# Performance work log

Hardware: AMD Instinct MI355X
Metric: run time of the kernel (lower is better)

## Reference

```python
import jax, jax.numpy as jnp
import numpy as np
from jax import lax

B, T, H, W, D = 4, 24, 32, 32, 128
N_CONV = 5            # 32 -> 1 via five stride-2 convs
NUM_FREQS = T // 2    # 12
N_EXPERTS = 7         # unique int periods of rfftfreq(24)[1:]
TOP_K = 2
BN_EPS = 1e-5
COMBINE_EPS = float(np.finfo(np.float64).eps)


def setup_inputs() -> dict:
    key = jax.random.key(0)
    ks = jax.random.split(key, 12)
    x = jax.random.normal(ks[0], (B, T, H, W, D), jnp.float32)
    conv_w = jax.random.normal(ks[1], (N_CONV, D, D, 2, 2), jnp.float32) / np.sqrt(4 * D)
    conv_b = jax.random.normal(ks[2], (N_CONV, D), jnp.float32) * 0.1
    bn_gamma = jax.random.uniform(ks[3], (N_CONV, D), jnp.float32, 0.5, 1.5)
    bn_beta = jax.random.normal(ks[4], (N_CONV, D), jnp.float32) * 0.1
    bn_mean = jax.random.normal(ks[5], (N_CONV, D), jnp.float32) * 0.1
    bn_var = jax.random.uniform(ks[6], (N_CONV, D), jnp.float32, 0.5, 1.5)
    fuse_w = jax.random.normal(ks[7], (D, 1), jnp.float32) / np.sqrt(D)
    fuse_b = jax.random.normal(ks[8], (1,), jnp.float32) * 0.1
    w_gate = jax.random.normal(ks[9], (NUM_FREQS, N_EXPERTS), jnp.float32)
    expert_w = jax.random.normal(ks[10], (N_EXPERTS, D, D), jnp.float32) / np.sqrt(D)
    expert_b = jax.random.normal(ks[11], (N_EXPERTS, D), jnp.float32) * 0.1
    return dict(x=x, conv_w=conv_w, conv_b=conv_b, bn_gamma=bn_gamma, bn_beta=bn_beta,
                bn_mean=bn_mean, bn_var=bn_var, fuse_w=fuse_w, fuse_b=fuse_b,
                w_gate=w_gate, expert_w=expert_w, expert_b=expert_b, top_k=TOP_K)


def _gates(x, conv_w, conv_b, bn_gamma, bn_beta, bn_mean, bn_var, fuse_w, fuse_b, w_gate, top_k):
    b, t, h, w, d = x.shape
    # (b t h w d) -> (bt, d, h, w)
    z = jnp.transpose(x.reshape(b * t, h, w, d), (0, 3, 1, 2))
    for i in range(conv_w.shape[0]):  # fixed small layer loop
        z = lax.conv_general_dilated(z, conv_w[i], (2, 2), 'VALID',
                                     dimension_numbers=('NCHW', 'OIHW', 'NCHW'))
        z = z + conv_b[i][None, :, None, None]
        z = bn_gamma[i][None, :, None, None] * (z - bn_mean[i][None, :, None, None]) \
            * lax.rsqrt(bn_var[i][None, :, None, None] + BN_EPS) + bn_beta[i][None, :, None, None]
        z = jnp.where(z > 0, z, 0.2 * z)  # LeakyReLU(0.2)
    hh, ww = z.shape[-2], z.shape[-1]
    # (bt, d, h, w) -> (b, t, h*w*d)  matching einops '(b t) d h w -> b t (h w d)'
    z = jnp.transpose(z.reshape(b, t, d, hh, ww), (0, 1, 3, 4, 2)).reshape(b, t, hh * ww * d)
    s = (z @ fuse_w + fuse_b)[..., 0]  # [B, T]
    xf = jnp.fft.rfft(s, axis=-1, norm='ortho')[:, 1:]  # drop DC -> [B, T//2]
    amp = jnp.abs(xf)
    logits = amp @ w_gate  # [B, E]  (eval path: no noise)
    top_vals, top_idx = lax.top_k(logits, top_k + 1)
    tk_vals, tk_idx = top_vals[:, :top_k], top_idx[:, :top_k]
    tk_gates = jax.nn.softmax(tk_vals, axis=-1)
    gates = jnp.zeros_like(logits).at[jnp.arange(b)[:, None], tk_idx].set(tk_gates)
    return gates


def reference(x, conv_w, conv_b, bn_gamma, bn_beta, bn_mean, bn_var,
              fuse_w, fuse_b, w_gate, expert_w, expert_b, top_k):
    gates = _gates(x, conv_w, conv_b, bn_gamma, bn_beta, bn_mean, bn_var,
                   fuse_w, fuse_b, w_gate, top_k)  # [B, E]
    # Dense equivalent of dispatch -> per-expert linear -> combine:
    # combine does exp(expert_out), gate-weighted scatter-add over batch, then log.
    expert_out = jnp.einsum('bthwd,edf->bethwf', x, expert_w) \
                 + expert_b[None, :, None, None, None, :]  # [B,E,T,H,W,D]
    combined = jnp.einsum('be,bethwf->bthwf', gates, jnp.exp(expert_out))
    combined = jnp.where(combined == 0, COMBINE_EPS, combined)
    return jnp.log(combined)
```

## Files before the change

### kernel.cpp

```cpp
#include <hip/hip_runtime.h>
#include <hip/hip_bf16.h>

#define D_ 128
#define T_ 24
#define NPB 24576

typedef __attribute__((ext_vector_type(8))) short bf16x8;
typedef __attribute__((ext_vector_type(4))) float f32x4;
typedef unsigned short ushortt;

static __device__ __forceinline__ void load8(const float* p, float* dst){
  float4 a = *(const float4*)p; float4 b = *(const float4*)(p+4);
  dst[0]=a.x;dst[1]=a.y;dst[2]=a.z;dst[3]=a.w;dst[4]=b.x;dst[5]=b.y;dst[6]=b.z;dst[7]=b.w;
}
static __device__ __forceinline__ bf16x8 cvt8(const float* f){
  union { bf16x8 v; __hip_bfloat162 h[4]; } u;
#pragma unroll
  for (int i=0;i<4;i++) u.h[i] = __float22bfloat162_rn(make_float2(f[2*i], f[2*i+1]));
  return u.v;
}
static __device__ __forceinline__ void split8(const float* f, bf16x8* hh, bf16x8* ll){
  union { bf16x8 v; __hip_bfloat162 h[4]; } uh, ul;
  float lo[8];
#pragma unroll
  for (int i=0;i<4;i++){
    __hip_bfloat162 p = __float22bfloat162_rn(make_float2(f[2*i], f[2*i+1]));
    uh.h[i] = p;
    lo[2*i]   = f[2*i]   - __bfloat162float(p.x);
    lo[2*i+1] = f[2*i+1] - __bfloat162float(p.y);
  }
#pragma unroll
  for (int i=0;i<4;i++) ul.h[i] = __float22bfloat162_rn(make_float2(lo[2*i], lo[2*i+1]));
  *hh = uh.v; *ll = ul.v;
}

__global__ void prep_frags(const float* __restrict__ cw, const float* __restrict__ ew,
                           ushortt* __restrict__ wfC, ushortt* __restrict__ wfE, int do_e)
{
  const int idx = blockIdx.x*256 + threadIdx.x;
  if (idx < 10240){
    const int l  = idx >> 11;
    const int n  = (idx >> 4) & 127;
    const int k8 = (idx & 15) * 8;
    const float* src = cw + (size_t)((l*128 + n)*128 + k8)*4;
    float4 v[8];
#pragma unroll
    for (int kk=0;kk<8;++kk) v[kk] = *(const float4*)&src[kk*4];
    const int fk = k8>>5, q = (k8>>3)&3, ng = n>>4;
    const int lanoff = (q*16 + (n&15))*8;
#pragma unroll
    for (int tap=0; tap<4; ++tap){
      float f[8];
#pragma unroll
      for (int kk=0;kk<8;++kk) f[kk] = ((const float*)&v[kk])[tap];
      bf16x8 hh, ll; split8(f, &hh, &ll);
      *(bf16x8*)&wfC[(size_t)((((l*4+tap)*2+0)*4+fk)*8+ng)*512 + lanoff] = hh;
      *(bf16x8*)&wfC[(size_t)((((l*4+tap)*2+1)*4+fk)*8+ng)*512 + lanoff] = ll;
    }
  } else if (do_e && idx < 10240 + 14336){
    const int j  = idx - 10240;
    const int e  = j >> 11;
    const int n  = (j >> 4) & 127;
    const int k8 = (j & 15) * 8;
    float f[8];
#pragma unroll
    for (int kk=0;kk<8;++kk) f[kk] = ew[(size_t)(e*128 + k8+kk)*128 + n];
    const int fk = k8>>5, q = (k8>>3)&3, ng = n>>4;
    *(bf16x8*)&wfE[(size_t)((e*4+fk)*8+ng)*512 + (q*16 + (n&15))*8] = cvt8(f);
  }
}

template<int MG>
__global__ __launch_bounds__(256, 4)
void conv3(const float* __restrict__ in, float* __restrict__ out,
           const ushortt* __restrict__ wf,
           const float* __restrict__ cb,  const float* __restrict__ gam,
           const float* __restrict__ bet, const float* __restrict__ mn,
           const float* __restrict__ vr,  int n_pix, int lw)
{
  const int t = threadIdx.x;
  const int w = t>>6, lane = t&63, quad = lane>>4, l16 = lane&15;
  const int nh = w*32;
  const int row0 = blockIdx.x*(MG*16);
  const int Win = 2<<lw;
  int inb[MG];
#pragma unroll
  for (int mg=0; mg<MG; ++mg){
    const int p = row0 + mg*16 + l16;
    const int n   = p >> (2*lw);
    const int rem = p - (n << (2*lw));
    const int oy  = rem >> lw, ox = rem - (oy<<lw);
    inb[mg] = ((n*Win  + 2*oy)*Win + 2*ox) << 7;
  }
  f32x4 acc[MG][2];
#pragma unroll
  for (int mg=0;mg<MG;++mg){ acc[mg][0]=(f32x4){0,0,0,0}; acc[mg][1]=acc[mg][0]; }

#pragma unroll
  for (int tap=0; tap<4; ++tap){
    const int toff = (((tap>>1)*Win) + (tap&1)) << 7;
#pragma unroll
    for (int fk=0; fk<4; ++fk){
      bf16x8 ah[MG], al[MG];
#pragma unroll
      for (int mg=0; mg<MG; ++mg){
        float f[8]; load8(in + inb[mg] + toff + fk*32 + quad*8, f);
        split8(f, &ah[mg], &al[mg]);
      }
#pragma unroll
      for (int ngl=0; ngl<2; ++ngl){
        const int ng = w*2 + ngl;
        const bf16x8 bh = *(const bf16x8*)&wf[(size_t)(((tap*2+0)*4+fk)*8+ng)*512 + lane*8];
        const bf16x8 bl = *(const bf16x8*)&wf[(size_t)(((tap*2+1)*4+fk)*8+ng)*512 + lane*8];
#pragma unroll
        for (int mg=0; mg<MG; ++mg){
          acc[mg][ngl] = __builtin_amdgcn_mfma_f32_16x16x32_bf16(ah[mg], bh, acc[mg][ngl], 0,0,0);
          acc[mg][ngl] = __builtin_amdgcn_mfma_f32_16x16x32_bf16(ah[mg], bl, acc[mg][ngl], 0,0,0);
          acc[mg][ngl] = __builtin_amdgcn_mfma_f32_16x16x32_bf16(al[mg], bh, acc[mg][ngl], 0,0,0);
        }
      }
    }
  }
#pragma unroll
  for (int ngl=0; ngl<2; ++ngl){
    const int col = nh + ngl*16 + l16;
    const float sc  = gam[col]*rsqrtf(vr[col]+1e-5f);
    const float cbv = cb[col], bt = bet[col], mv = mn[col];
#pragma unroll
    for (int mg=0; mg<MG; ++mg)
#pragma unroll
      for (int r=0; r<4; ++r){
        const int pix = row0 + mg*16 + quad*4 + r;
        float v = acc[mg][ngl][r] + cbv;
        v = sc*(v - mv) + bt;
        out[(size_t)pix*D_ + col] = v>0.f ? v : 0.2f*v;
      }
  }
}

__global__ void gate_kernel(const float* __restrict__ z, const float* __restrict__ fw,
                            const float* __restrict__ fb, const float* __restrict__ wg,
                            float* __restrict__ gbuf)
{
  __shared__ float s[96];
  __shared__ float amp[4][12];
  __shared__ float logits[4][7];
  const int t = threadIdx.x;
  if (t < 96){
    float a = 0.f;
    for (int d=0; d<D_; d++) a = fmaf(z[t*D_+d], fw[d], a);
    s[t] = a + fb[0];
  }
  __syncthreads();
  if (t < 48){
    const int b = t / 12, kf = (t % 12) + 1;
    float re=0.f, im=0.f;
    for (int tt=0; tt<T_; tt++){
      int ph = (kf*tt) % T_;
      float ang = (float)ph * (6.283185307179586f / (float)T_);
      re = fmaf(s[b*T_+tt], cosf(ang), re);
      im = fmaf(s[b*T_+tt], sinf(ang), im);
    }
    amp[b][t%12] = sqrtf(re*re + im*im) * 0.20412414523193150f;
  }
  __syncthreads();
  if (t < 28){
    const int b = t/7, e = t - (t/7)*7;
    float a = 0.f;
    for (int k=0;k<12;k++) a = fmaf(amp[b][k], wg[k*7+e], a);
    logits[b][e] = a;
  }
  __syncthreads();
  if (t < 4){
    const int b = t;
    int i0=0; float v0=logits[b][0];
    for (int e=1;e<7;e++){ float v=logits[b][e]; if (v > v0){ v0=v; i0=e; } }
    int i1=-1; float v1=-3.4e38f;
    for (int e=0;e<7;e++){ if (e==i0) continue; float v=logits[b][e]; if (v > v1){ v1=v; i1=e; } }
    float ed = expf(v1 - v0);
    gbuf[b*4+0] = 1.f/(1.f+ed);
    gbuf[b*4+1] = ed/(1.f+ed);
    ((int*)gbuf)[b*4+2] = i0;
    ((int*)gbuf)[b*4+3] = i1;
  }
}

template<bool WF>
__global__ __launch_bounds__(256, 3)
void expert3(const float* __restrict__ x, const float* __restrict__ ew,
             const ushortt* __restrict__ wfe, const float* __restrict__ eb,
             const float* __restrict__ gbuf, float* __restrict__ outp)
{
  __shared__ ushortt wlds[WF ? 16 : 32768];
  const int t = threadIdx.x;
  const int w = t>>6, lane = t&63, quad = lane>>4, l16 = lane&15;
  const int nh = w*32;
  const size_t row0 = (size_t)blockIdx.x * 64;
  const int b = (int)(row0 / NPB);
  const float g0 = gbuf[b*4+0], g1 = gbuf[b*4+1];
  const int e0 = ((const int*)gbuf)[b*4+2];
  const int e1 = ((const int*)gbuf)[b*4+3];

  if (!WF){
    const int el = t>>7, r7 = t&127;
    const int n0 = (r7&31)*4, k0 = (r7>>5)*16;
    const int esel = el ? e1 : e0;
#pragma unroll
    for (int h=0; h<2; ++h)
#pragma unroll
      for (int sub=0; sub<2; ++sub){
        const int kb = h*64 + k0 + sub*8;
        float4 v[8];
#pragma unroll
        for (int kk=0;kk<8;++kk)
          v[kk] = *(const float4*)&ew[(size_t)esel*16384 + (size_t)(kb+kk)*D_ + n0];
        const int fk = kb>>5, q = (kb>>3)&3;
#pragma unroll
        for (int n=0;n<4;++n){
          float f[8];
#pragma unroll
          for (int kk=0;kk<8;++kk) f[kk] = ((const float*)&v[kk])[n];
          *(bf16x8*)&wlds[(size_t)(((el*4+fk)*8 + ((n0+n)>>4))*512 + (q*16 + ((n0+n)&15))*8)] = cvt8(f);
        }
      }
    __syncthreads();
  }

  f32x4 acc[2][4][2];
#pragma unroll
  for (int e=0;e<2;++e)
#pragma unroll
    for (int mg=0;mg<4;++mg){ acc[e][mg][0]=(f32x4){0,0,0,0}; acc[e][mg][1]=acc[e][mg][0]; }

#pragma unroll
  for (int fk=0; fk<4; ++fk){
    bf16x8 a[4];
#pragma unroll
    for (int mg=0; mg<4; ++mg){
      float f[8]; load8(x + (row0 + mg*16 + l16)*D_ + fk*32 + quad*8, f);
      a[mg] = cvt8(f);
    }
#pragma unroll
    for (int e=0; e<2; ++e){
      const int eg = e ? e1 : e0;
#pragma unroll
      for (int ngl=0; ngl<2; ++ngl){
        const int ng = w*2 + ngl;
        bf16x8 bb;
        if (WF) bb = *(const bf16x8*)&wfe[(size_t)((eg*4+fk)*8+ng)*512 + lane*8];
        else    bb = *(const bf16x8*)&wlds[(size_t)((e*4+fk)*8+ng)*512 + lane*8];
#pragma unroll
        for (int mg=0; mg<4; ++mg)
          acc[e][mg][ngl] = __builtin_amdgcn_mfma_f32_16x16x32_bf16(a[mg], bb, acc[e][mg][ngl], 0,0,0);
      }
    }
  }
#pragma unroll
  for (int ngl=0; ngl<2; ++ngl){
    const int col = nh + ngl*16 + l16;
    const float be0 = eb[e0*D_ + col];
    const float be1 = eb[e1*D_ + col];
#pragma unroll
    for (int mg=0; mg<4; ++mg)
#pragma unroll
      for (int r=0; r<4; ++r){
        const size_t row = row0 + mg*16 + quad*4 + r;
        float c = g0*__expf(acc[0][mg][ngl][r] + be0) + g1*__expf(acc[1][mg][ngl][r] + be1);
        if (c == 0.f) c = 2.220446049250313e-16f;
        outp[row*D_ + col] = __logf(c);
      }
  }
}

extern "C" void kernel_launch(void* const* d_in, const int* in_sizes, int n_in,
                              void* d_out, int out_size, void* d_ws, size_t ws_size,
                              hipStream_t stream)
{
  const float* x   = (const float*)d_in[0];
  const float* cw  = (const float*)d_in[1];
  const float* cb  = (const float*)d_in[2];
  const float* gam = (const float*)d_in[3];
  const float* bet = (const float*)d_in[4];
  const float* mn  = (const float*)d_in[5];
  const float* vr  = (const float*)d_in[6];
  const float* fw  = (const float*)d_in[7];
  const float* fb  = (const float*)d_in[8];
  const float* wg  = (const float*)d_in[9];
  const float* ew  = (const float*)d_in[10];
  const float* eb  = (const float*)d_in[11];
  float* out = (float*)d_out;

  char* sb = (char*)d_out;
  ushortt* wfC = (ushortt*)sb;
  float* bufA  = (float*)(sb + 1310720);
  float* bufB  = (float*)(sb + 13893632);
  float* zbuf  = (float*)(sb + 17039360);
  float* gbuf  = (float*)d_ws;

  const bool use_wf = ws_size >= (size_t)(64 + 7*4*8*512*2);
  ushortt* wfE = use_wf ? (ushortt*)((char*)d_ws + 64) : wfC ;

  prep_frags<<<96, 256, 0, stream>>>(cw, ew, wfC, wfE, use_wf ? 1 : 0);
  conv3<2><<<768, 256, 0, stream>>>(x,    bufA, wfC,          cb,     gam,     bet,     mn,     vr,     24576, 4);
  conv3<2><<<192, 256, 0, stream>>>(bufA, bufB, wfC + 131072, cb+128, gam+128, bet+128, mn+128, vr+128,  6144, 3);
  conv3<1><<< 96, 256, 0, stream>>>(bufB, bufA, wfC + 262144, cb+256, gam+256, bet+256, mn+256, vr+256,  1536, 2);
  conv3<1><<< 24, 256, 0, stream>>>(bufA, bufB, wfC + 393216, cb+384, gam+384, bet+384, mn+384, vr+384,   384, 1);
  conv3<1><<<  6, 256, 0, stream>>>(bufB, zbuf, wfC + 524288, cb+512, gam+512, bet+512, mn+512, vr+512,    96, 0);
  gate_kernel<<<1, 128, 0, stream>>>(zbuf, fw, fb, wg, gbuf);
  if (use_wf) expert3<true ><<<1536, 256, 0, stream>>>(x, ew, wfE, eb, gbuf, out);
  else        expert3<false><<<1536, 256, 0, stream>>>(x, ew, wfE, eb, gbuf, out);
}
```

Before: 223.0 us.

## Fuse all stages into one cooperative persistent kernel with grid syncs

After: 222.9 us. Within noise of the previous version (-0.0%).

```diff
diff --git a/kernel.cpp b/kernel.cpp
--- a/kernel.cpp
+++ b/kernel.cpp
@@ -1,5 +1,8 @@
 #include <hip/hip_runtime.h>
 #include <hip/hip_bf16.h>
+#include <hip/hip_cooperative_groups.h>
+
+namespace cg = cooperative_groups;
 
 #define D_ 128
 #define T_ 24
@@ -34,10 +37,10 @@
   *hh = uh.v; *ll = ul.v;
 }
 
-__global__ void prep_frags(const float* __restrict__ cw, const float* __restrict__ ew,
-                           ushortt* __restrict__ wfC, ushortt* __restrict__ wfE, int do_e)
-{
-  const int idx = blockIdx.x*256 + threadIdx.x;
+static __device__ __forceinline__ void prep_body(const float* __restrict__ cw,
+    const float* __restrict__ ew, ushortt* __restrict__ wfC, ushortt* __restrict__ wfE,
+    int do_e, int idx)
+{
   if (idx < 10240){
     const int l  = idx >> 11;
     const int n  = (idx >> 4) & 127;
@@ -70,6 +73,78 @@
   }
 }
 
+__global__ void prep_frags(const float* __restrict__ cw, const float* __restrict__ ew,
+                           ushortt* __restrict__ wfC, ushortt* __restrict__ wfE, int do_e)
+{
+  prep_body(cw, ew, wfC, wfE, do_e, blockIdx.x*256 + threadIdx.x);
+}
+
+template<int MG>
+static __device__ __forceinline__ void conv_body(const float* __restrict__ in,
+           float* __restrict__ out, const ushortt* __restrict__ wf,
+           const float* __restrict__ cb,  const float* __restrict__ gam,
+           const float* __restrict__ bet, const float* __restrict__ mn,
+           const float* __restrict__ vr,  int row0, int lw)
+{
+  const int t = threadIdx.x;
+  const int w = t>>6, lane = t&63, quad = lane>>4, l16 = lane&15;
+  const int nh = w*32;
+  const int Win = 2<<lw;
+  int inb[MG];
+#pragma unroll
+  for (int mg=0; mg<MG; ++mg){
+    const int p = row0 + mg*16 + l16;
+    const int n   = p >> (2*lw);
+    const int rem = p - (n << (2*lw));
+    const int oy  = rem >> lw, ox = rem - (oy<<lw);
+    inb[mg] = ((n*Win  + 2*oy)*Win + 2*ox) << 7;
+  }
+  f32x4 acc[MG][2];
+#pragma unroll
+  for (int mg=0;mg<MG;++mg){ acc[mg][0]=(f32x4){0,0,0,0}; acc[mg][1]=acc[mg][0]; }
+
+#pragma unroll
+  for (int tap=0; tap<4; ++tap){
+    const int toff = (((tap>>1)*Win) + (tap&1)) << 7;
+#pragma unroll
+    for (int fk=0; fk<4; ++fk){
+      bf16x8 ah[MG], al[MG];
+#pragma unroll
+      for (int mg=0; mg<MG; ++mg){
+        float f[8]; load8(in + inb[mg] + toff + fk*32 + quad*8, f);
+        split8(f, &ah[mg], &al[mg]);
+      }
+#pragma unroll
+      for (int ngl=0; ngl<2; ++ngl){
+        const int ng = w*2 + ngl;
+        const bf16x8 bh = *(const bf16x8*)&wf[(size_t)(((tap*2+0)*4+fk)*8+ng)*512 + lane*8];
+        const bf16x8 bl = *(const bf16x8*)&wf[(size_t)(((tap*2+1)*4+fk)*8+ng)*512 + lane*8];
+#pragma unroll
+        for (int mg=0; mg<MG; ++mg){
+          acc[mg][ngl] = __builtin_amdgcn_mfma_f32_16x16x32_bf16(ah[mg], bh, acc[mg][ngl], 0,0,0);
+          acc[mg][ngl] = __builtin_amdgcn_mfma_f32_16x16x32_bf16(ah[mg], bl, acc[mg][ngl], 0,0,0);
+          acc[mg][ngl] = __builtin_amdgcn_mfma_f32_16x16x32_bf16(al[mg], bh, acc[mg][ngl], 0,0,0);
+        }
+      }
+    }
+  }
+#pragma unroll
+  for (int ngl=0; ngl<2; ++ngl){
+    const int col = nh + ngl*16 + l16;
+    const float sc  = gam[col]*rsqrtf(vr[col]+1e-5f);
+    const float cbv = cb[col], bt = bet[col], mv = mn[col];
+#pragma unroll
+    for (int mg=0; mg<MG; ++mg)
+#pragma unroll
+      for (int r=0; r<4; ++r){
+        const int pix = row0 + mg*16 + quad*4 + r;
+        float v = acc[mg][ngl][r] + cbv;
+        v = sc*(v - mv) + bt;
+        out[(size_t)pix*D_ + col] = v>0.f ? v : 0.2f*v;
+      }
+  }
+}
+
 template<int MG>
 __global__ __launch_bounds__(256, 4)
 void conv3(const float* __restrict__ in, float* __restrict__ out,
@@ -78,69 +153,13 @@
            const float* __restrict__ bet, const float* __restrict__ mn,
            const float* __restrict__ vr,  int n_pix, int lw)
 {
-  const int t = threadIdx.x;
-  const int w = t>>6, lane = t&63, quad = lane>>4, l16 = lane&15;
-  const int nh = w*32;
-  const int row0 = blockIdx.x*(MG*16);
-  const int Win = 2<<lw;
-  int inb[MG];
-#pragma unroll
-  for (int mg=0; mg<MG; ++mg){
-    const int p = row0 + mg*16 + l16;
-    const int n   = p >> (2*lw);
-    const int rem = p - (n << (2*lw));
-    const int oy  = rem >> lw, ox = rem - (oy<<lw);
-    inb[mg] = ((n*Win  + 2*oy)*Win + 2*ox) << 7;
-  }
-  f32x4 acc[MG][2];
-#pragma unroll
-  for (int mg=0;mg<MG;++mg){ acc[mg][0]=(f32x4){0,0,0,0}; acc[mg][1]=acc[mg][0]; }
-
-#pragma unroll
-  for (int tap=0; tap<4; ++tap){
-    const int toff = (((tap>>1)*Win) + (tap&1)) << 7;
-#pragma unroll
-    for (int fk=0; fk<4; ++fk){
-      bf16x8 ah[MG], al[MG];
-#pragma unroll
-      for (int mg=0; mg<MG; ++mg){
-        float f[8]; load8(in + inb[mg] + toff + fk*32 + quad*8, f);
-        split8(f, &ah[mg], &al[mg]);
-      }
-#pragma unroll
-      for (int ngl=0; ngl<2; ++ngl){
-        const int ng = w*2 + ngl;
-        const bf16x8 bh = *(const bf16x8*)&wf[(size_t)(((tap*2+0)*4+fk)*8+ng)*512 + lane*8];
-        const bf16x8 bl = *(const bf16x8*)&wf[(size_t)(((tap*2+1)*4+fk)*8+ng)*512 + lane*8];
-#pragma unroll
-        for (int mg=0; mg<MG; ++mg){
-          acc[mg][ngl] = __builtin_amdgcn_mfma_f32_16x16x32_bf16(ah[mg], bh, acc[mg][ngl], 0,0,0);
-          acc[mg][ngl] = __builtin_amdgcn_mfma_f32_16x16x32_bf16(ah[mg], bl, acc[mg][ngl], 0,0,0);
-          acc[mg][ngl] = __builtin_amdgcn_mfma_f32_16x16x32_bf16(al[mg], bh, acc[mg][ngl], 0,0,0);
-        }
-      }
-    }
-  }
-#pragma unroll
-  for (int ngl=0; ngl<2; ++ngl){
-    const int col = nh + ngl*16 + l16;
-    const float sc  = gam[col]*rsqrtf(vr[col]+1e-5f);
-    const float cbv = cb[col], bt = bet[col], mv = mn[col];
-#pragma unroll
-    for (int mg=0; mg<MG; ++mg)
-#pragma unroll
-      for (int r=0; r<4; ++r){
-        const int pix = row0 + mg*16 + quad*4 + r;
-        float v = acc[mg][ngl][r] + cbv;
-        v = sc*(v - mv) + bt;
-        out[(size_t)pix*D_ + col] = v>0.f ? v : 0.2f*v;
-      }
-  }
-}
-
-__global__ void gate_kernel(const float* __restrict__ z, const float* __restrict__ fw,
-                            const float* __restrict__ fb, const float* __restrict__ wg,
-                            float* __restrict__ gbuf)
+  (void)n_pix;
+  conv_body<MG>(in, out, wf, cb, gam, bet, mn, vr, blockIdx.x*(MG*16), lw);
+}
+
+static __device__ __forceinline__ void gate_body(const float* __restrict__ z,
+    const float* __restrict__ fw, const float* __restrict__ fb,
+    const float* __restrict__ wg, float* __restrict__ gbuf)
 {
   __shared__ float s[96];
   __shared__ float amp[4][12];
@@ -185,91 +204,145 @@
   }
 }
 
+__global__ void gate_kernel(const float* __restrict__ z, const float* __restrict__ fw,
+                            const float* __restrict__ fb, const float* __restrict__ wg,
+                            float* __restrict__ gbuf)
+{
+  gate_body(z, fw, fb, wg, gbuf);
+}
+
+template<bool WF>
+static __device__ __forceinline__ void expert_tile(const float* __restrict__ x,
+             const float* __restrict__ ew, const ushortt* __restrict__ wfe,
+             const float* __restrict__ eb, const float* __restrict__ gbuf,
+             float* __restrict__ outp, size_t row0)
+{
+  __shared__ ushortt wlds[WF ? 16 : 32768];
+  const int t = threadIdx.x;
+  const int w = t>>6, lane = t&63, quad = lane>>4, l16 = lane&15;
+  const int nh = w*32;
+  const int b = (int)(row0 / NPB);
+  const float g0 = gbuf[b*4+0], g1 = gbuf[b*4+1];
+  const int e0 = ((const int*)gbuf)[b*4+2];
+  const int e1 = ((const int*)gbuf)[b*4+3];
+
+  if (!WF){
+    const int el = t>>7, r7 = t&127;
+    const int n0 = (r7&31)*4, k0 = (r7>>5)*16;
+    const int esel = el ? e1 : e0;
+#pragma unroll
+    for (int h=0; h<2; ++h)
+#pragma unroll
+      for (int sub=0; sub<2; ++sub){
+        const int kb = h*64 + k0 + sub*8;
+        float4 v[8];
+#pragma unroll
+        for (int kk=0;kk<8;++kk)
+          v[kk] = *(const float4*)&ew[(size_t)esel*16384 + (size_t)(kb+kk)*D_ + n0];
+        const int fk = kb>>5, q = (kb>>3)&3;
+#pragma unroll
+        for (int n=0;n<4;++n){
+          float f[8];
+#pragma unroll
+          for (int kk=0;kk<8;++kk) f[kk] = ((const float*)&v[kk])[n];
+          *(bf16x8*)&wlds[(size_t)(((el*4+fk)*8 + ((n0+n)>>4))*512 + (q*16 + ((n0+n)&15))*8)] = cvt8(f);
+        }
+      }
+    __syncthreads();
+  }
+
+  f32x4 acc[2][4][2];
+#pragma unroll
+  for (int e=0;e<2;++e)
+#pragma unroll
+    for (int mg=0;mg<4;++mg){ acc[e][mg][0]=(f32x4){0,0,0,0}; acc[e][mg][1]=acc[e][mg][0]; }
+
+#pragma unroll
+  for (int fk=0; fk<4; ++fk){
+    bf16x8 a[4];
+#pragma unroll
+    for (int mg=0; mg<4; ++mg){
+      float f[8]; load8(x + (row0 + mg*16 + l16)*D_ + fk*32 + quad*8, f);
+      a[mg] = cvt8(f);
+    }
+#pragma unroll
+    for (int e=0; e<2; ++e){
+      const int eg = e ? e1 : e0;
+#pragma unroll
+      for (int ngl=0; ngl<2; ++ngl){
+        const int ng = w*2 + ngl;
+        bf16x8 bb;
+        if (WF) bb = *(const bf16x8*)&wfe[(size_t)((eg*4+fk)*8+ng)*512 + lane*8];
+        else    bb = *(const bf16x8*)&wlds[(size_t)((e*4+fk)*8+ng)*512 + lane*8];
+#pragma unroll
+        for (int mg=0; mg<4; ++mg)
+          acc[e][mg][ngl] = __builtin_amdgcn_mfma_f32_16x16x32_bf16(a[mg], bb, acc[e][mg][ngl], 0,0,0);
+      }
+    }
+  }
+#pragma unroll
+  for (int ngl=0; ngl<2; ++ngl){
+    const int col = nh + ngl*16 + l16;
+    const float be0 = eb[e0*D_ + col];
+    const float be1 = eb[e1*D_ + col];
+#pragma unroll
+    for (int mg=0; mg<4; ++mg)
+#pragma unroll
+      for (int r=0; r<4; ++r){
+        const size_t row = row0 + mg*16 + quad*4 + r;
+        float c = g0*__expf(acc[0][mg][ngl][r] + be0) + g1*__expf(acc[1][mg][ngl][r] + be1);
+        if (c == 0.f) c = 2.220446049250313e-16f;
+        outp[row*D_ + col] = __logf(c);
+      }
+  }
+}
+
 template<bool WF>
 __global__ __launch_bounds__(256, 3)
 void expert3(const float* __restrict__ x, const float* __restrict__ ew,
              const ushortt* __restrict__ wfe, const float* __restrict__ eb,
              const float* __restrict__ gbuf, float* __restrict__ outp)
 {
-  __shared__ ushortt wlds[WF ? 16 : 32768];
-  const int t = threadIdx.x;
-  const int w = t>>6, lane = t&63, quad = lane>>4, l16 = lane&15;
-  const int nh = w*32;
-  const size_t row0 = (size_t)blockIdx.x * 64;
-  const int b = (int)(row0 / NPB);
-  const float g0 = gbuf[b*4+0], g1 = gbuf[b*4+1];
-  const int e0 = ((const int*)gbuf)[b*4+2];
-  const int e1 = ((const int*)gbuf)[b*4+3];
-
-  if (!WF){
-    const int el = t>>7, r7 = t&127;
-    const int n0 = (r7&31)*4, k0 = (r7>>5)*16;
-    const int esel = el ? e1 : e0;
-#pragma unroll
-    for (int h=0; h<2; ++h)
-#pragma unroll
-      for (int sub=0; sub<2; ++sub){
-        const int kb = h*64 + k0 + sub*8;
-        float4 v[8];
-#pragma unroll
-        for (int kk=0;kk<8;++kk)
-          v[kk] = *(const float4*)&ew[(size_t)esel*16384 + (size_t)(kb+kk)*D_ + n0];
-        const int fk = kb>>5, q = (kb>>3)&3;
-#pragma unroll
-        for (int n=0;n<4;++n){
-          float f[8];
-#pragma unroll
-          for (int kk=0;kk<8;++kk) f[kk] = ((const float*)&v[kk])[n];
-          *(bf16x8*)&wlds[(size_t)(((el*4+fk)*8 + ((n0+n)>>4))*512 + (q*16 + ((n0+n)&15))*8)] = cvt8(f);
-        }
-      }
-    __syncthreads();
-  }
-
-  f32x4 acc[2][4][2];
-#pragma unroll
-  for (int e=0;e<2;++e)
-#pragma unroll
-    for (int mg=0;mg<4;++mg){ acc[e][mg][0]=(f32x4){0,0,0,0}; acc[e][mg][1]=acc[e][mg][0]; }
-
-#pragma unroll
-  for (int fk=0; fk<4; ++fk){
-    bf16x8 a[4];
-#pragma unroll
-    for (int mg=0; mg<4; ++mg){
-      float f[8]; load8(x + (row0 + mg*16 + l16)*D_ + fk*32 + quad*8, f);
-      a[mg] = cvt8(f);
-    }
-#pragma unroll
-    for (int e=0; e<2; ++e){
-      const int eg = e ? e1 : e0;
-#pragma unroll
-      for (int ngl=0; ngl<2; ++ngl){
-        const int ng = w*2 + ngl;
-        bf16x8 bb;
-        if (WF) bb = *(const bf16x8*)&wfe[(size_t)((eg*4+fk)*8+ng)*512 + lane*8];
-        else    bb = *(const bf16x8*)&wlds[(size_t)((e*4+fk)*8+ng)*512 + lane*8];
-#pragma unroll
-        for (int mg=0; mg<4; ++mg)
-          acc[e][mg][ngl] = __builtin_amdgcn_mfma_f32_16x16x32_bf16(a[mg], bb, acc[e][mg][ngl], 0,0,0);
-      }
-    }
-  }
-#pragma unroll
-  for (int ngl=0; ngl<2; ++ngl){
-    const int col = nh + ngl*16 + l16;
-    const float be0 = eb[e0*D_ + col];
-    const float be1 = eb[e1*D_ + col];
-#pragma unroll
-    for (int mg=0; mg<4; ++mg)
-#pragma unroll
-      for (int r=0; r<4; ++r){
-        const size_t row = row0 + mg*16 + quad*4 + r;
-        float c = g0*__expf(acc[0][mg][ngl][r] + be0) + g1*__expf(acc[1][mg][ngl][r] + be1);
-        if (c == 0.f) c = 2.220446049250313e-16f;
-        outp[row*D_ + col] = __logf(c);
-      }
-  }
+  expert_tile<WF>(x, ew, wfe, eb, gbuf, outp, (size_t)blockIdx.x * 64);
+}
+
+__global__ __launch_bounds__(256, 3)
+void mega(const float* __restrict__ x,  const float* __restrict__ cw,
+          const float* __restrict__ ew, const float* __restrict__ cb,
+          const float* __restrict__ gam,const float* __restrict__ bet,
+          const float* __restrict__ mn, const float* __restrict__ vr,
+          const float* __restrict__ fw, const float* __restrict__ fb,
+          const float* __restrict__ wg, const float* __restrict__ eb,
+          float* __restrict__ outbase,  float* __restrict__ gbuf,
+          ushortt* __restrict__ wfE)
+{
+  cg::grid_group grid = cg::this_grid();
+  char* sb = (char*)outbase;
+  ushortt* wfC = (ushortt*)sb;
+  float* bufA  = (float*)(sb + 1310720);
+  float* bufB  = (float*)(sb + 13893632);
+  float* zbuf  = (float*)(sb + 17039360);
+
+  prep_body(cw, ew, wfC, wfE, 1, blockIdx.x*256 + threadIdx.x);
+  grid.sync();
+  conv_body<2>(x, bufA, wfC, cb, gam, bet, mn, vr, blockIdx.x*32, 4);
+  grid.sync();
+  if (blockIdx.x < 384)
+    conv_body<1>(bufA, bufB, wfC+131072, cb+128, gam+128, bet+128, mn+128, vr+128, blockIdx.x*16, 3);
+  grid.sync();
+  if (blockIdx.x < 96)
+    conv_body<1>(bufB, bufA, wfC+262144, cb+256, gam+256, bet+256, mn+256, vr+256, blockIdx.x*16, 2);
+  grid.sync();
+  if (blockIdx.x < 24)
+    conv_body<1>(bufA, bufB, wfC+393216, cb+384, gam+384, bet+384, mn+384, vr+384, blockIdx.x*16, 1);
+  grid.sync();
+  if (blockIdx.x < 6)
+    conv_body<1>(bufB, zbuf, wfC+524288, cb+512, gam+512, bet+512, mn+512, vr+512, blockIdx.x*16, 0);
+  grid.sync();
+  if (blockIdx.x == 0) gate_body(zbuf, fw, fb, wg, gbuf);
+  grid.sync();
+  expert_tile<true>(x, ew, wfE, eb, gbuf, outbase, (size_t)blockIdx.x * 64);
+  expert_tile<true>(x, ew, wfE, eb, gbuf, outbase, (size_t)(blockIdx.x + 768) * 64);
 }
 
 extern "C" void kernel_launch(void* const* d_in, const int* in_sizes, int n_in,
@@ -300,6 +373,24 @@
   const bool use_wf = ws_size >= (size_t)(64 + 7*4*8*512*2);
   ushortt* wfE = use_wf ? (ushortt*)((char*)d_ws + 64) : wfC ;
 
+  static int coop_ok = -1;
+  if (coop_ok < 0){
+    int mb = 0;
+    hipError_t e = hipOccupancyMaxActiveBlocksPerMultiprocessor(&mb, (const void*)mega, 256, 0);
+    coop_ok = (e == hipSuccess && mb >= 3) ? 1 : 0;
+  }
+
+  if (use_wf && coop_ok == 1){
+    void* args[] = { (void*)&x, (void*)&cw, (void*)&ew, (void*)&cb, (void*)&gam, (void*)&bet,
+                     (void*)&mn, (void*)&vr, (void*)&fw, (void*)&fb, (void*)&wg, (void*)&eb,
+                     (void*)&out, (void*)&gbuf, (void*)&wfE };
+    hipError_t err = hipLaunchCooperativeKernel((const void*)mega, dim3(768), dim3(256),
+                                                args, 0, stream);
+    if (err == hipSuccess) return;
+    (void)hipGetLastError();
+    coop_ok = 0;
+  }
+
   prep_frags<<<96, 256, 0, stream>>>(cw, ew, wfC, wfE, use_wf ? 1 : 0);
   conv3<2><<<768, 256, 0, stream>>>(x,    bufA, wfC,          cb,     gam,     bet,     mn,     vr,     24576, 4);
   conv3<2><<<192, 256, 0, stream>>>(bufA, bufB, wfC + 131072, cb+128, gam+128, bet+128, mn+128, vr+128,  6144, 3);
```

## Fuse conv stages 2-5 into one LDS-resident kernel and fold gating into expert

Applied to the files above, without the earlier changes.

Result: no change. 223.1 us (+0.1%).

```diff
diff --git a/kernel.cpp b/kernel.cpp
--- a/kernel.cpp
+++ b/kernel.cpp
@@ -4,6 +4,7 @@
 #define D_ 128
 #define T_ 24
 #define NPB 24576
+#define TSTR 132
 
 typedef __attribute__((ext_vector_type(8))) short bf16x8;
 typedef __attribute__((ext_vector_type(4))) float f32x4;
@@ -78,6 +79,7 @@
            const float* __restrict__ bet, const float* __restrict__ mn,
            const float* __restrict__ vr,  int n_pix, int lw)
 {
+  (void)n_pix;
   const int t = threadIdx.x;
   const int w = t>>6, lane = t&63, quad = lane>>4, l16 = lane&15;
   const int nh = w*32;
@@ -136,6 +138,136 @@
         out[(size_t)pix*D_ + col] = v>0.f ? v : 0.2f*v;
       }
   }
+}
+
+template<int WOUT>
+static __device__ __forceinline__ void stage_lds(const float* __restrict__ sIn,
+    float* __restrict__ sOut, float* __restrict__ gOut,
+    const ushortt* __restrict__ wf,
+    const float* __restrict__ cb, const float* __restrict__ gam,
+    const float* __restrict__ bet, const float* __restrict__ mn,
+    const float* __restrict__ vr, int t)
+{
+  const int w = t>>6, lane = t&63, quad = lane>>4, l16 = lane&15;
+  const int nh = w*32;
+  const int R  = WOUT*WOUT;
+  const int Wi = 2*WOUT;
+  const int p  = (l16 < R) ? l16 : 0;
+  const int oy = (WOUT==4) ? (p>>2) : (WOUT==2 ? (p>>1) : 0);
+  const int ox = (WOUT==4) ? (p&3)  : (WOUT==2 ? (p&1)  : 0);
+  const int inb = 2*oy*Wi + 2*ox;
+  f32x4 acc[2];
+  acc[0]=(f32x4){0,0,0,0}; acc[1]=acc[0];
+#pragma unroll
+  for (int tap=0; tap<4; ++tap){
+    const int toff = (tap>>1)*Wi + (tap&1);
+#pragma unroll
+    for (int fk=0; fk<4; ++fk){
+      float f[8]; load8(sIn + (size_t)(inb+toff)*TSTR + fk*32 + quad*8, f);
+      bf16x8 ah, al; split8(f, &ah, &al);
+#pragma unroll
+      for (int ngl=0; ngl<2; ++ngl){
+        const int ng = w*2 + ngl;
+        const bf16x8 bh = *(const bf16x8*)&wf[(size_t)(((tap*2+0)*4+fk)*8+ng)*512 + lane*8];
+        const bf16x8 bl = *(const bf16x8*)&wf[(size_t)(((tap*2+1)*4+fk)*8+ng)*512 + lane*8];
+        acc[ngl] = __builtin_amdgcn_mfma_f32_16x16x32_bf16(ah, bh, acc[ngl], 0,0,0);
+        acc[ngl] = __builtin_amdgcn_mfma_f32_16x16x32_bf16(ah, bl, acc[ngl], 0,0,0);
+        acc[ngl] = __builtin_amdgcn_mfma_f32_16x16x32_bf16(al, bh, acc[ngl], 0,0,0);
+      }
+    }
+  }
+#pragma unroll
+  for (int ngl=0; ngl<2; ++ngl){
+    const int col = nh + ngl*16 + l16;
+    const float sc  = gam[col]*rsqrtf(vr[col]+1e-5f);
+    const float cbv = cb[col], btv = bet[col], mv = mn[col];
+#pragma unroll
+    for (int r=0; r<4; ++r){
+      const int row = quad*4 + r;
+      if (row < R){
+        float v = acc[ngl][r] + cbv;
+        v = sc*(v - mv) + btv;
+        v = v>0.f ? v : 0.2f*v;
+        if (WOUT > 1) sOut[(size_t)row*TSTR + col] = v;
+        else          gOut[col] = v;
+      }
+    }
+  }
+}
+
+__global__ __launch_bounds__(256, 2)
+void tail_kernel(const float* __restrict__ bufA, const ushortt* __restrict__ wfC,
+                 const float* __restrict__ cb,  const float* __restrict__ gam,
+                 const float* __restrict__ bet, const float* __restrict__ mn,
+                 const float* __restrict__ vr,  float* __restrict__ zbuf)
+{
+  __shared__ float sA[64*TSTR];
+  __shared__ float sB[16*TSTR];
+  __shared__ float sC[ 4*TSTR];
+  const int bt = blockIdx.x;
+  const int t = threadIdx.x;
+  const int w = t>>6, lane = t&63, quad = lane>>4, l16 = lane&15;
+  const int nh = w*32;
+
+  {
+    const ushortt* wf = wfC + 131072;
+    int inb[4];
+#pragma unroll
+    for (int mg=0; mg<4; ++mg){
+      const int p = mg*16 + l16;
+      const int oy = p>>3, ox = p&7;
+      inb[mg] = ((bt*16 + 2*oy)*16 + 2*ox) << 7;
+    }
+    f32x4 acc[4][2];
+#pragma unroll
+    for (int mg=0;mg<4;++mg){ acc[mg][0]=(f32x4){0,0,0,0}; acc[mg][1]=acc[mg][0]; }
+#pragma unroll
+    for (int tap=0; tap<4; ++tap){
+      const int toff = (((tap>>1)*16) + (tap&1)) << 7;
+#pragma unroll
+      for (int fk=0; fk<4; ++fk){
+        bf16x8 ah[4], al[4];
+#pragma unroll
+        for (int mg=0; mg<4; ++mg){
+          float f[8]; load8(bufA + (size_t)inb[mg] + toff + fk*32 + quad*8, f);
+          split8(f, &ah[mg], &al[mg]);
+        }
+#pragma unroll
+        for (int ngl=0; ngl<2; ++ngl){
+          const int ng = w*2 + ngl;
+          const bf16x8 bh = *(const bf16x8*)&wf[(size_t)(((tap*2+0)*4+fk)*8+ng)*512 + lane*8];
+          const bf16x8 bl = *(const bf16x8*)&wf[(size_t)(((tap*2+1)*4+fk)*8+ng)*512 + lane*8];
+#pragma unroll
+          for (int mg=0; mg<4; ++mg){
+            acc[mg][ngl] = __builtin_amdgcn_mfma_f32_16x16x32_bf16(ah[mg], bh, acc[mg][ngl], 0,0,0);
+            acc[mg][ngl] = __builtin_amdgcn_mfma_f32_16x16x32_bf16(ah[mg], bl, acc[mg][ngl], 0,0,0);
+            acc[mg][ngl] = __builtin_amdgcn_mfma_f32_16x16x32_bf16(al[mg], bh, acc[mg][ngl], 0,0,0);
+          }
+        }
+      }
+    }
+#pragma unroll
+    for (int ngl=0; ngl<2; ++ngl){
+      const int col = nh + ngl*16 + l16;
+      const float sc  = gam[128+col]*rsqrtf(vr[128+col]+1e-5f);
+      const float cbv = cb[128+col], btv = bet[128+col], mv = mn[128+col];
+#pragma unroll
+      for (int mg=0; mg<4; ++mg)
+#pragma unroll
+        for (int r=0; r<4; ++r){
+          const int row = mg*16 + quad*4 + r;
+          float v = acc[mg][ngl][r] + cbv;
+          v = sc*(v - mv) + btv;
+          sA[(size_t)row*TSTR + col] = v>0.f ? v : 0.2f*v;
+        }
+    }
+  }
+  __syncthreads();
+  stage_lds<4>(sA, sB, nullptr, wfC + 262144, cb+256, gam+256, bet+256, mn+256, vr+256, t);
+  __syncthreads();
+  stage_lds<2>(sB, sC, nullptr, wfC + 393216, cb+384, gam+384, bet+384, mn+384, vr+384, t);
+  __syncthreads();
+  stage_lds<1>(sC, nullptr, zbuf + (size_t)bt*D_, wfC + 524288, cb+512, gam+512, bet+512, mn+512, vr+512, t);
 }
 
 __global__ void gate_kernel(const float* __restrict__ z, const float* __restrict__ fw,
@@ -182,6 +314,106 @@
     gbuf[b*4+1] = ed/(1.f+ed);
     ((int*)gbuf)[b*4+2] = i0;
     ((int*)gbuf)[b*4+3] = i1;
+  }
+}
+
+__global__ __launch_bounds__(256, 3)
+void expert_gate(const float* __restrict__ x, const ushortt* __restrict__ wfe,
+                 const float* __restrict__ eb, const float* __restrict__ zbuf,
+                 const float* __restrict__ fw, const float* __restrict__ fb,
+                 const float* __restrict__ wg, float* __restrict__ outp)
+{
+  __shared__ float ssig[T_];
+  __shared__ float samp[12];
+  __shared__ float slog[7];
+  __shared__ float sg[2];
+  __shared__ int   se[2];
+  const int t = threadIdx.x;
+  const int w = t>>6, lane = t&63, quad = lane>>4, l16 = lane&15;
+  const int nh = w*32;
+  const size_t row0 = (size_t)blockIdx.x * 64;
+  const int b = (int)(row0 / NPB);
+
+  if (t < T_){
+    const float* zr = zbuf + (size_t)(b*T_ + t)*D_;
+    float a = 0.f;
+    for (int d=0; d<D_; d++) a = fmaf(zr[d], fw[d], a);
+    ssig[t] = a + fb[0];
+  }
+  __syncthreads();
+  if (t < 12){
+    const int kf = t + 1;
+    float re=0.f, im=0.f;
+    for (int tt=0; tt<T_; tt++){
+      int ph = (kf*tt) % T_;
+      float ang = (float)ph * (6.283185307179586f / (float)T_);
+      re = fmaf(ssig[tt], cosf(ang), re);
+      im = fmaf(ssig[tt], sinf(ang), im);
+    }
+    samp[t] = sqrtf(re*re + im*im) * 0.20412414523193150f;
+  }
+  __syncthreads();
+  if (t < 7){
+    float a = 0.f;
+    for (int k=0;k<12;k++) a = fmaf(samp[k], wg[k*7+t], a);
+    slog[t] = a;
+  }
+  __syncthreads();
+  if (t == 0){
+    int i0=0; float v0=slog[0];
+    for (int e=1;e<7;e++){ float v=slog[e]; if (v > v0){ v0=v; i0=e; } }
+    int i1=-1; float v1=-3.4e38f;
+    for (int e=0;e<7;e++){ if (e==i0) continue; float v=slog[e]; if (v > v1){ v1=v; i1=e; } }
+    float ed = expf(v1 - v0);
+    sg[0] = 1.f/(1.f+ed);
+    sg[1] = ed/(1.f+ed);
+    se[0] = i0; se[1] = i1;
+  }
+  __syncthreads();
+  const float g0 = sg[0], g1 = sg[1];
+  const int e0 = se[0], e1 = se[1];
+
+  f32x4 acc[2][4][2];
+#pragma unroll
+  for (int e=0;e<2;++e)
+#pragma unroll
+    for (int mg=0;mg<4;++mg){ acc[e][mg][0]=(f32x4){0,0,0,0}; acc[e][mg][1]=acc[e][mg][0]; }
+
+#pragma unroll
+  for (int fk=0; fk<4; ++fk){
+    bf16x8 a[4];
+#pragma unroll
+    for (int mg=0; mg<4; ++mg){
+      float f[8]; load8(x + (row0 + mg*16 + l16)*D_ + fk*32 + quad*8, f);
+      a[mg] = cvt8(f);
+    }
+#pragma unroll
+    for (int e=0; e<2; ++e){
+      const int eg = e ? e1 : e0;
+#pragma unroll
+      for (int ngl=0; ngl<2; ++ngl){
+        const int ng = w*2 + ngl;
+        const bf16x8 bb = *(const bf16x8*)&wfe[(size_t)((eg*4+fk)*8+ng)*512 + lane*8];
+#pragma unroll
+        for (int mg=0; mg<4; ++mg)
+          acc[e][mg][ngl] = __builtin_amdgcn_mfma_f32_16x16x32_bf16(a[mg], bb, acc[e][mg][ngl], 0,0,0);
+      }
+    }
+  }
+#pragma unroll
+  for (int ngl=0; ngl<2; ++ngl){
+    const int col = nh + ngl*16 + l16;
+    const float be0 = eb[e0*D_ + col];
+    const float be1 = eb[e1*D_ + col];
+#pragma unroll
+    for (int mg=0; mg<4; ++mg)
+#pragma unroll
+      for (int r=0; r<4; ++r){
+        const size_t row = row0 + mg*16 + quad*4 + r;
+        float c = g0*__expf(acc[0][mg][ngl][r] + be0) + g1*__expf(acc[1][mg][ngl][r] + be1);
+        if (c == 0.f) c = 2.220446049250313e-16f;
+        outp[row*D_ + col] = __logf(c);
+      }
   }
 }
 
@@ -293,20 +525,33 @@
   char* sb = (char*)d_out;
   ushortt* wfC = (ushortt*)sb;
   float* bufA  = (float*)(sb + 1310720);
+
+  const size_t WFE_BYTES = (size_t)7*4*8*512*2;
+  const bool primary = ws_size >= WFE_BYTES + 96*D_*sizeof(float);
+  ushortt* wfE = (ushortt*)d_ws;
+  float* zbuf_ws = (float*)((char*)d_ws + WFE_BYTES);
+
+  if (primary){
+    prep_frags<<<96, 256, 0, stream>>>(cw, ew, wfC, wfE, 1);
+    conv3<2><<<768, 256, 0, stream>>>(x, bufA, wfC, cb, gam, bet, mn, vr, 24576, 4);
+    tail_kernel<<<96, 256, 0, stream>>>(bufA, wfC, cb, gam, bet, mn, vr, zbuf_ws);
+    expert_gate<<<1536, 256, 0, stream>>>(x, wfE, eb, zbuf_ws, fw, fb, wg, out);
+    return;
+  }
+
   float* bufB  = (float*)(sb + 13893632);
   float* zbuf  = (float*)(sb + 17039360);
   float* gbuf  = (float*)d_ws;
-
-  const bool use_wf = ws_size >= (size_t)(64 + 7*4*8*512*2);
-  ushortt* wfE = use_wf ? (ushortt*)((char*)d_ws + 64) : wfC ;
-
-  prep_frags<<<96, 256, 0, stream>>>(cw, ew, wfC, wfE, use_wf ? 1 : 0);
+  const bool use_wf = ws_size >= (size_t)(64 + WFE_BYTES);
+  ushortt* wfE2 = use_wf ? (ushortt*)((char*)d_ws + 64) : wfC;
+
+  prep_frags<<<96, 256, 0, stream>>>(cw, ew, wfC, wfE2, use_wf ? 1 : 0);
   conv3<2><<<768, 256, 0, stream>>>(x,    bufA, wfC,          cb,     gam,     bet,     mn,     vr,     24576, 4);
   conv3<2><<<192, 256, 0, stream>>>(bufA, bufB, wfC + 131072, cb+128, gam+128, bet+128, mn+128, vr+128,  6144, 3);
   conv3<1><<< 96, 256, 0, stream>>>(bufB, bufA, wfC + 262144, cb+256, gam+256, bet+256, mn+256, vr+256,  1536, 2);
   conv3<1><<< 24, 256, 0, stream>>>(bufA, bufB, wfC + 393216, cb+384, gam+384, bet+384, mn+384, vr+384,   384, 1);
   conv3<1><<<  6, 256, 0, stream>>>(bufB, zbuf, wfC + 524288, cb+512, gam+512, bet+512, mn+512, vr+512,    96, 0);
   gate_kernel<<<1, 128, 0, stream>>>(zbuf, fw, fb, wg, gbuf);
-  if (use_wf) expert3<true ><<<1536, 256, 0, stream>>>(x, ew, wfE, eb, gbuf, out);
-  else        expert3<false><<<1536, 256, 0, stream>>>(x, ew, wfE, eb, gbuf, out);
-}
+  if (use_wf) expert3<true ><<<1536, 256, 0, stream>>>(x, ew, wfE2, eb, gbuf, out);
+  else        expert3<false><<<1536, 256, 0, stream>>>(x, ew, wfE2, eb, gbuf, out);
+}
```
